# Kernel optimization log

Hardware: AMD Instinct MI355X
Metric: run time of the kernel (lower is better)

The kernel has to match this reference:

```python
import jax, jax.numpy as jnp
import numpy as np

B, T, I, H, O = 512, 1024, 15, 64, 11

def setup_inputs() -> dict:
    key = jax.random.key(0)
    ks = jax.random.split(key, 7)
    s_ih = 1.0 / np.sqrt(H)
    return {
        "x": jax.random.normal(ks[0], (B, T, I), dtype=jnp.float32),
        # torch nn.RNN params: weight_ih_l0 [H,I], weight_hh_l0 [H,H], biases [H]
        "W_ih": jax.random.uniform(ks[1], (H, I), jnp.float32, -s_ih, s_ih),
        "b_ih": jax.random.uniform(ks[2], (H,), jnp.float32, -s_ih, s_ih),
        "W_hh": jax.random.uniform(ks[3], (H, H), jnp.float32, -s_ih, s_ih),
        "b_hh": jax.random.uniform(ks[4], (H,), jnp.float32, -s_ih, s_ih),
        # decoder Linear(64, 11)
        "W_dec": jax.random.uniform(ks[5], (O, H), jnp.float32, -s_ih, s_ih),
        "b_dec": jax.random.uniform(ks[6], (O,), jnp.float32, -s_ih, s_ih),
    }

def reference(x, W_ih, b_ih, W_hh, b_hh, W_dec, b_dec):
    # Precompute input projection for all timesteps: [T, B, H]
    xproj = jnp.einsum("bti,hi->tbh", x, W_ih) + b_ih + b_hh
    h0 = jnp.zeros((x.shape[0], W_hh.shape[0]), dtype=x.dtype)

    def step(h, xp_t):
        h_new = jax.nn.relu(xp_t + h @ W_hh.T)  # [B, H]
        return h_new, h_new

    h_last, hs = jax.lax.scan(step, h0, xproj)  # hs: [T, B, H]
    out_seq = jnp.transpose(hs, (1, 0, 2))       # [B, T, H]
    out = jax.nn.relu(jnp.einsum("bth,oh->bto", out_seq, W_dec) + b_dec)
    h = h_last[None]  # [1, B, H] matching torch num_layers dim
    return (out, h)
```

## Files before the change

kernel.cpp:

```cpp
#include <hip/hip_runtime.h>
#include <hip/hip_fp16.h>
#include <stdint.h>

#define BB 512
#define TT 1024
#define II 15
#define HH 64
#define OO 11

typedef __fp16 half2v __attribute__((ext_vector_type(2)));
typedef _Float16 half8 __attribute__((ext_vector_type(8)));
typedef float floatx4 __attribute__((ext_vector_type(4)));
typedef int int4v __attribute__((ext_vector_type(4)));

union PK { int i; half2v h; float f; };

__device__ __forceinline__ half2v i2h2(int v) { PK u; u.i = v; return u.h; }
__device__ __forceinline__ int h22i(half2v v) { PK u; u.h = v; return u.i; }

__device__ __forceinline__ float FDOT2(half2v a, half2v b, float c) {
    return __builtin_amdgcn_fdot2(a, b, c, false);
}

__device__ __forceinline__ float lane_xor1(float v) {
    PK u; u.f = v;
    u.i = __builtin_amdgcn_mov_dpp(u.i, 0xB1, 0xF, 0xF, false);
    return u.f;
}

__global__ __launch_bounds__(64) void rnn_rec(
    const float* __restrict__ x, const float* __restrict__ W_ih,
    const float* __restrict__ b_ih, const float* __restrict__ W_hh,
    const float* __restrict__ b_hh, _Float16* __restrict__ hs,
    float* __restrict__ h_last)
{
    __shared__ __align__(16) int xbuf[2][64 * 8];
    __shared__ __align__(16) _Float16 hbuf[64];
    const int b = blockIdx.x;
    const int lane = threadIdx.x;

    half2v whh[32];
#pragma unroll
    for (int p = 0; p < 32; ++p)
        whh[p] = __builtin_amdgcn_cvt_pkrtz(W_hh[lane * HH + 2 * p],
                                            W_hh[lane * HH + 2 * p + 1]);
    half2v wx[8];
#pragma unroll
    for (int j = 0; j < 7; ++j)
        wx[j] = __builtin_amdgcn_cvt_pkrtz(W_ih[lane * II + 2 * j],
                                           W_ih[lane * II + 2 * j + 1]);
    wx[7] = __builtin_amdgcn_cvt_pkrtz(W_ih[lane * II + 14],
                                       b_ih[lane] + b_hh[lane]);

    const float* xb = x + (size_t)b * TT * II;
    _Float16* hrow = hs + (size_t)b * TT * HH + lane;
    const int4v* hb4 = (const int4v*)hbuf;

    {
        float cf[II];
#pragma unroll
        for (int i = 0; i < II; ++i) cf[i] = xb[lane * II + i];
        int4v p0, p1;
        p0.x = h22i(__builtin_amdgcn_cvt_pkrtz(cf[0], cf[1]));
        p0.y = h22i(__builtin_amdgcn_cvt_pkrtz(cf[2], cf[3]));
        p0.z = h22i(__builtin_amdgcn_cvt_pkrtz(cf[4], cf[5]));
        p0.w = h22i(__builtin_amdgcn_cvt_pkrtz(cf[6], cf[7]));
        p1.x = h22i(__builtin_amdgcn_cvt_pkrtz(cf[8], cf[9]));
        p1.y = h22i(__builtin_amdgcn_cvt_pkrtz(cf[10], cf[11]));
        p1.z = h22i(__builtin_amdgcn_cvt_pkrtz(cf[12], cf[13]));
        p1.w = h22i(__builtin_amdgcn_cvt_pkrtz(cf[14], 1.0f));
        *(int4v*)&xbuf[0][lane * 8] = p0;
        *(int4v*)&xbuf[0][lane * 8 + 4] = p1;
    }
    hbuf[lane] = (_Float16)0.0f;

    float xa[8];
    {
        const int4v xv0 = *(const int4v*)&xbuf[0][0];
        const int4v xv1 = *(const int4v*)&xbuf[0][4];
        xa[0] = FDOT2(i2h2(xv0.x), wx[0], 0.0f);
        xa[1] = FDOT2(i2h2(xv0.y), wx[1], 0.0f);
        xa[2] = FDOT2(i2h2(xv0.z), wx[2], 0.0f);
        xa[3] = FDOT2(i2h2(xv0.w), wx[3], 0.0f);
        xa[4] = FDOT2(i2h2(xv1.x), wx[4], 0.0f);
        xa[5] = FDOT2(i2h2(xv1.y), wx[5], 0.0f);
        xa[6] = FDOT2(i2h2(xv1.z), wx[6], 0.0f);
        xa[7] = FDOT2(i2h2(xv1.w), wx[7], 0.0f);
    }

    float h = 0.0f;
    int hpk = 0;

    auto step = [&](int t) {
        int4v hb[6];
#pragma unroll
        for (int q = 0; q < 6; ++q) hb[q] = hb4[q + 2];

        float a0 = xa[0], a1 = xa[1], a2 = xa[2], a3 = xa[3];
        float a4 = xa[4], a5 = xa[5], a6 = xa[6], a7 = xa[7];

        a0 = FDOT2(i2h2(__builtin_amdgcn_readlane(hpk, 0)),  whh[0], a0);
        a1 = FDOT2(i2h2(__builtin_amdgcn_readlane(hpk, 2)),  whh[1], a1);
        a2 = FDOT2(i2h2(__builtin_amdgcn_readlane(hpk, 4)),  whh[2], a2);
        a3 = FDOT2(i2h2(__builtin_amdgcn_readlane(hpk, 6)),  whh[3], a3);
        a4 = FDOT2(i2h2(__builtin_amdgcn_readlane(hpk, 8)),  whh[4], a4);
        a5 = FDOT2(i2h2(__builtin_amdgcn_readlane(hpk, 10)), whh[5], a5);
        a6 = FDOT2(i2h2(__builtin_amdgcn_readlane(hpk, 12)), whh[6], a6);
        a7 = FDOT2(i2h2(__builtin_amdgcn_readlane(hpk, 14)), whh[7], a7);

#pragma unroll
        for (int q = 0; q < 6; ++q) {
            const int base = 8 + 4 * q;
            if ((q & 1) == 0) {
                a0 = FDOT2(i2h2(hb[q].x), whh[base + 0], a0);
                a1 = FDOT2(i2h2(hb[q].y), whh[base + 1], a1);
                a2 = FDOT2(i2h2(hb[q].z), whh[base + 2], a2);
                a3 = FDOT2(i2h2(hb[q].w), whh[base + 3], a3);
            } else {
                a4 = FDOT2(i2h2(hb[q].x), whh[base + 0], a4);
                a5 = FDOT2(i2h2(hb[q].y), whh[base + 1], a5);
                a6 = FDOT2(i2h2(hb[q].z), whh[base + 2], a6);
                a7 = FDOT2(i2h2(hb[q].w), whh[base + 3], a7);
            }
        }
        h = fmaxf(((a0 + a1) + (a2 + a3)) + ((a4 + a5) + (a6 + a7)), 0.0f);
        const _Float16 hf = (_Float16)h;
        hbuf[lane] = hf;

        const int tn = t + 1;
        const int* xp = &xbuf[(tn >> 6) & 1][(tn & 63) * 8];
        const int4v xv0 = *(const int4v*)xp;
        const int4v xv1 = *(const int4v*)(xp + 4);

        hrow[(size_t)t * HH] = hf;

        hpk = h22i(__builtin_amdgcn_cvt_pkrtz(h, lane_xor1(h)));

        xa[0] = FDOT2(i2h2(xv0.x), wx[0], 0.0f);
        xa[1] = FDOT2(i2h2(xv0.y), wx[1], 0.0f);
        xa[2] = FDOT2(i2h2(xv0.z), wx[2], 0.0f);
        xa[3] = FDOT2(i2h2(xv0.w), wx[3], 0.0f);
        xa[4] = FDOT2(i2h2(xv1.x), wx[4], 0.0f);
        xa[5] = FDOT2(i2h2(xv1.y), wx[5], 0.0f);
        xa[6] = FDOT2(i2h2(xv1.z), wx[6], 0.0f);
        xa[7] = FDOT2(i2h2(xv1.w), wx[7], 0.0f);
    };

    for (int tc = 0; tc < TT; tc += 64) {
        const int tnb = (tc + 64 < TT) ? (tc + 64) : tc;
        float nf[II];
#pragma unroll
        for (int i = 0; i < II; ++i)
            nf[i] = xb[(size_t)(tnb + lane) * II + i];

        for (int to = 0; to < 32; to += 8)
#pragma unroll
            for (int u = 0; u < 8; ++u) step(tc + to + u);

        {
            const int cb = ((tc >> 6) + 1) & 1;
            int4v p0, p1;
            p0.x = h22i(__builtin_amdgcn_cvt_pkrtz(nf[0], nf[1]));
            p0.y = h22i(__builtin_amdgcn_cvt_pkrtz(nf[2], nf[3]));
            p0.z = h22i(__builtin_amdgcn_cvt_pkrtz(nf[4], nf[5]));
            p0.w = h22i(__builtin_amdgcn_cvt_pkrtz(nf[6], nf[7]));
            p1.x = h22i(__builtin_amdgcn_cvt_pkrtz(nf[8], nf[9]));
            p1.y = h22i(__builtin_amdgcn_cvt_pkrtz(nf[10], nf[11]));
            p1.z = h22i(__builtin_amdgcn_cvt_pkrtz(nf[12], nf[13]));
            p1.w = h22i(__builtin_amdgcn_cvt_pkrtz(nf[14], 1.0f));
            *(int4v*)&xbuf[cb][lane * 8] = p0;
            *(int4v*)&xbuf[cb][lane * 8 + 4] = p1;
        }

        for (int to = 32; to < 64; to += 8)
#pragma unroll
            for (int u = 0; u < 8; ++u) step(tc + to + u);
    }
    h_last[b * HH + lane] = h;
}

__global__ __launch_bounds__(256) void rnn_decode(
    const _Float16* __restrict__ hs, const float* __restrict__ W_dec,
    const float* __restrict__ b_dec, float* __restrict__ out)
{
    __shared__ __align__(16) _Float16 wl[16 * HH];
    const int tid = threadIdx.x;
    for (int i = tid; i < 16 * HH; i += 256)
        wl[i] = (_Float16)((i < OO * HH) ? W_dec[i] : 0.0f);
    __syncthreads();

    const int lane = tid & 63;
    const int wid  = tid >> 6;
    const int col  = lane & 15;
    const int quad = lane >> 4;
    const float bd = (col < OO) ? b_dec[col] : 0.0f;

    half8 bf0 = *(const half8*)&wl[col * HH + quad * 8];
    half8 bf1 = *(const half8*)&wl[col * HH + 32 + quad * 8];

    const size_t tile = (size_t)blockIdx.x * 4 + wid;
    const size_t btb = tile * 16;
    const _Float16* ap = hs + (btb + (size_t)col) * HH + quad * 8;
    half8 a0 = *(const half8*)ap;
    half8 a1 = *(const half8*)(ap + 32);

    floatx4 acc = {0.0f, 0.0f, 0.0f, 0.0f};
    acc = __builtin_amdgcn_mfma_f32_16x16x32_f16(a0, bf0, acc, 0, 0, 0);
    acc = __builtin_amdgcn_mfma_f32_16x16x32_f16(a1, bf1, acc, 0, 0, 0);

    if (col < OO) {
#pragma unroll
        for (int r = 0; r < 4; ++r) {
            const size_t row = btb + (size_t)(quad * 4 + r);
            out[row * OO + col] = fmaxf(acc[r] + bd, 0.0f);
        }
    }
}

extern "C" void kernel_launch(void* const* d_in, const int* in_sizes, int n_in,
                              void* d_out, int out_size, void* d_ws, size_t ws_size,
                              hipStream_t stream) {
    const float* x     = (const float*)d_in[0];
    const float* W_ih  = (const float*)d_in[1];
    const float* b_ih  = (const float*)d_in[2];
    const float* W_hh  = (const float*)d_in[3];
    const float* b_hh  = (const float*)d_in[4];
    const float* W_dec = (const float*)d_in[5];
    const float* b_dec = (const float*)d_in[6];

    float* out    = (float*)d_out;
    float* h_last = out + (size_t)BB * TT * OO;
    _Float16* hs  = (_Float16*)d_ws;

    rnn_rec<<<BB, 64, 0, stream>>>(x, W_ih, b_ih, W_hh, b_hh, hs, h_last);
    rnn_decode<<<8192, 256, 0, stream>>>(hs, W_dec, b_dec, out);
}
```

Before: 273.5 us.

## Fuse decoder projection into recurrent kernel, removing hidden-state workspace round trip

Computes the 64-to-11 decoder dot product inside the recurrence loop. Each group of four lanes reads the previous step's hidden vector from shared memory, does packed fp16 dot products and reduces with DPP shuffles. The output for step t-1 is stored during step t, and a final epilogue handles the last step. This drops the fp16 hidden-state writes to workspace and the separate MFMA decode launch, but adds about ten instructions plus two LDS loads to every serial recurrence step.

```diff
diff --git a/kernel.cpp b/kernel.cpp
--- a/kernel.cpp
+++ b/kernel.cpp
@@ -9,7 +9,6 @@
 #define OO 11
 
 typedef __fp16 half2v __attribute__((ext_vector_type(2)));
-typedef _Float16 half8 __attribute__((ext_vector_type(8)));
 typedef float floatx4 __attribute__((ext_vector_type(4)));
 typedef int int4v __attribute__((ext_vector_type(4)));
 
@@ -28,10 +27,17 @@
     return u.f;
 }
 
+__device__ __forceinline__ float lane_xor2(float v) {
+    PK u; u.f = v;
+    u.i = __builtin_amdgcn_mov_dpp(u.i, 0x4E, 0xF, 0xF, false);
+    return u.f;
+}
+
 __global__ __launch_bounds__(64) void rnn_rec(
     const float* __restrict__ x, const float* __restrict__ W_ih,
     const float* __restrict__ b_ih, const float* __restrict__ W_hh,
-    const float* __restrict__ b_hh, _Float16* __restrict__ hs,
+    const float* __restrict__ b_hh, const float* __restrict__ W_dec,
+    const float* __restrict__ b_dec, float* __restrict__ out,
     float* __restrict__ h_last)
 {
     __shared__ __align__(16) int xbuf[2][64 * 8];
@@ -52,8 +58,19 @@
     wx[7] = __builtin_amdgcn_cvt_pkrtz(W_ih[lane * II + 14],
                                        b_ih[lane] + b_hh[lane]);
 
+    const int od = lane >> 2;
+    const int oc = (od < OO) ? od : 0;
+    const int ks = lane & 3;
+    half2v wdec[8];
+#pragma unroll
+    for (int p = 0; p < 8; ++p)
+        wdec[p] = __builtin_amdgcn_cvt_pkrtz(W_dec[oc * HH + (ks * 8 + p) * 2],
+                                             W_dec[oc * HH + (ks * 8 + p) * 2 + 1]);
+    const float bd = b_dec[oc];
+    const bool dostore = (ks == 0) && (od < OO);
+    float* outb = out + (size_t)b * TT * OO + od;
+
     const float* xb = x + (size_t)b * TT * II;
-    _Float16* hrow = hs + (size_t)b * TT * HH + lane;
     const int4v* hb4 = (const int4v*)hbuf;
 
     {
@@ -92,6 +109,9 @@
     int hpk = 0;
 
     auto step = [&](int t) {
+        const int4v d0 = *(const int4v*)((const char*)hbuf + ks * 32);
+        const int4v d1 = *(const int4v*)((const char*)hbuf + ks * 32 + 16);
+
         int4v hb[6];
 #pragma unroll
         for (int q = 0; q < 6; ++q) hb[q] = hb4[q + 2];
@@ -132,7 +152,20 @@
         const int4v xv0 = *(const int4v*)xp;
         const int4v xv1 = *(const int4v*)(xp + 4);
 
-        hrow[(size_t)t * HH] = hf;
+        float dacc = FDOT2(i2h2(d0.x), wdec[0], 0.0f);
+        dacc = FDOT2(i2h2(d0.y), wdec[1], dacc);
+        dacc = FDOT2(i2h2(d0.z), wdec[2], dacc);
+        dacc = FDOT2(i2h2(d0.w), wdec[3], dacc);
+        dacc = FDOT2(i2h2(d1.x), wdec[4], dacc);
+        dacc = FDOT2(i2h2(d1.y), wdec[5], dacc);
+        dacc = FDOT2(i2h2(d1.z), wdec[6], dacc);
+        dacc = FDOT2(i2h2(d1.w), wdec[7], dacc);
+        dacc += lane_xor1(dacc);
+        dacc += lane_xor2(dacc);
+        if (dostore) {
+            const int tm = (t > 0) ? (t - 1) : 0;
+            outb[(size_t)tm * OO] = fmaxf(dacc + bd, 0.0f);
+        }
 
         hpk = h22i(__builtin_amdgcn_cvt_pkrtz(h, lane_xor1(h)));
 
@@ -176,45 +209,25 @@
 #pragma unroll
             for (int u = 0; u < 8; ++u) step(tc + to + u);
     }
+
+    {
+        const int4v d0 = *(const int4v*)((const char*)hbuf + ks * 32);
+        const int4v d1 = *(const int4v*)((const char*)hbuf + ks * 32 + 16);
+        float dacc = FDOT2(i2h2(d0.x), wdec[0], 0.0f);
+        dacc = FDOT2(i2h2(d0.y), wdec[1], dacc);
+        dacc = FDOT2(i2h2(d0.z), wdec[2], dacc);
+        dacc = FDOT2(i2h2(d0.w), wdec[3], dacc);
+        dacc = FDOT2(i2h2(d1.x), wdec[4], dacc);
+        dacc = FDOT2(i2h2(d1.y), wdec[5], dacc);
+        dacc = FDOT2(i2h2(d1.z), wdec[6], dacc);
+        dacc = FDOT2(i2h2(d1.w), wdec[7], dacc);
+        dacc += lane_xor1(dacc);
+        dacc += lane_xor2(dacc);
+        if (dostore)
+            outb[(size_t)(TT - 1) * OO] = fmaxf(dacc + bd, 0.0f);
+    }
+
     h_last[b * HH + lane] = h;
-}
-
-__global__ __launch_bounds__(256) void rnn_decode(
-    const _Float16* __restrict__ hs, const float* __restrict__ W_dec,
-    const float* __restrict__ b_dec, float* __restrict__ out)
-{
-    __shared__ __align__(16) _Float16 wl[16 * HH];
-    const int tid = threadIdx.x;
-    for (int i = tid; i < 16 * HH; i += 256)
-        wl[i] = (_Float16)((i < OO * HH) ? W_dec[i] : 0.0f);
-    __syncthreads();
-
-    const int lane = tid & 63;
-    const int wid  = tid >> 6;
-    const int col  = lane & 15;
-    const int quad = lane >> 4;
-    const float bd = (col < OO) ? b_dec[col] : 0.0f;
-
-    half8 bf0 = *(const half8*)&wl[col * HH + quad * 8];
-    half8 bf1 = *(const half8*)&wl[col * HH + 32 + quad * 8];
-
-    const size_t tile = (size_t)blockIdx.x * 4 + wid;
-    const size_t btb = tile * 16;
-    const _Float16* ap = hs + (btb + (size_t)col) * HH + quad * 8;
-    half8 a0 = *(const half8*)ap;
-    half8 a1 = *(const half8*)(ap + 32);
-
-    floatx4 acc = {0.0f, 0.0f, 0.0f, 0.0f};
-    acc = __builtin_amdgcn_mfma_f32_16x16x32_f16(a0, bf0, acc, 0, 0, 0);
-    acc = __builtin_amdgcn_mfma_f32_16x16x32_f16(a1, bf1, acc, 0, 0, 0);
-
-    if (col < OO) {
-#pragma unroll
-        for (int r = 0; r < 4; ++r) {
-            const size_t row = btb + (size_t)(quad * 4 + r);
-            out[row * OO + col] = fmaxf(acc[r] + bd, 0.0f);
-        }
-    }
 }
 
 extern "C" void kernel_launch(void* const* d_in, const int* in_sizes, int n_in,
@@ -230,8 +243,7 @@
 
     float* out    = (float*)d_out;
     float* h_last = out + (size_t)BB * TT * OO;
-    _Float16* hs  = (_Float16*)d_ws;
-
-    rnn_rec<<<BB, 64, 0, stream>>>(x, W_ih, b_ih, W_hh, b_hh, hs, h_last);
-    rnn_decode<<<8192, 256, 0, stream>>>(hs, W_dec, b_dec, out);
-}
+
+    rnn_rec<<<BB, 64, 0, stream>>>(x, W_ih, b_ih, W_hh, b_hh,
+                                   W_dec, b_dec, out, h_last);
+}
```

Result: slower. 336.2 us (+23.0%).
